# Kernel optimization log

Hardware: AMD Instinct MI355X
Metric: run time of the kernel (lower is better)

## Reference

```python
import jax, jax.numpy as jnp
import numpy as np

N, E, D_IN, D_H, D_OUT = 50000, 640000, 128, 128, 64
EPS = 1e-5


def _sage(x, src, dst, Wl, bl, Wr):
    # PyG SAGEConv: out = lin_l(mean_{j in N(i)} x_j) + lin_r(x_i)
    msg = x[src]                                             # [E, d] gather
    agg = jax.ops.segment_sum(msg, dst, num_segments=x.shape[0])
    deg = jax.ops.segment_sum(jnp.ones((src.shape[0],), x.dtype), dst,
                              num_segments=x.shape[0])
    agg = agg / jnp.maximum(deg, 1.0)[:, None]               # mean aggregate
    return agg @ Wl + bl + x @ Wr


def _bn_eval(x, gamma, beta, mean, var):
    return (x - mean) * jax.lax.rsqrt(var + EPS) * gamma + beta


def setup_inputs() -> dict:
    key = jax.random.key(0)
    ks = jax.random.split(key, 16)
    s = lambda d: 1.0 / np.sqrt(d)
    inp = {
        "x": jax.random.normal(ks[0], (N, D_IN), jnp.float32),
        "edge_index": jax.random.randint(ks[1], (2, E), 0, N, jnp.int64),
        # layer 0: 128 -> 128
        "Wl0": jax.random.normal(ks[2], (D_IN, D_H), jnp.float32) * s(D_IN),
        "bl0": jnp.zeros((D_H,), jnp.float32),
        "Wr0": jax.random.normal(ks[3], (D_IN, D_H), jnp.float32) * s(D_IN),
        # layer 1: 128 -> 128
        "Wl1": jax.random.normal(ks[4], (D_H, D_H), jnp.float32) * s(D_H),
        "bl1": jnp.zeros((D_H,), jnp.float32),
        "Wr1": jax.random.normal(ks[5], (D_H, D_H), jnp.float32) * s(D_H),
        # layer 2: 128 -> 64
        "Wl2": jax.random.normal(ks[6], (D_H, D_OUT), jnp.float32) * s(D_H),
        "bl2": jnp.zeros((D_OUT,), jnp.float32),
        "Wr2": jax.random.normal(ks[7], (D_H, D_OUT), jnp.float32) * s(D_H),
        # BatchNorm (eval mode) for the two hidden layers
        "g0": jnp.ones((D_H,), jnp.float32),
        "b0": jnp.zeros((D_H,), jnp.float32),
        "m0": jax.random.normal(ks[8], (D_H,), jnp.float32) * 0.1,
        "v0": jax.random.uniform(ks[9], (D_H,), jnp.float32, 0.5, 1.5),
        "g1": jnp.ones((D_H,), jnp.float32),
        "b1": jnp.zeros((D_H,), jnp.float32),
        "m1": jax.random.normal(ks[10], (D_H,), jnp.float32) * 0.1,
        "v1": jax.random.uniform(ks[11], (D_H,), jnp.float32, 0.5, 1.5),
    }
    return inp


def reference(x, edge_index, Wl0, bl0, Wr0, Wl1, bl1, Wr1, Wl2, bl2, Wr2,
              g0, b0, m0, v0, g1, b1, m1, v1):
    src, dst = edge_index[0], edge_index[1]
    # edge mask (edge_index < N) is all-true by construction -> no-op
    h = _sage(x, src, dst, Wl0, bl0, Wr0)
    h = jax.nn.relu(_bn_eval(h, g0, b0, m0, v0))   # eval: dropout is identity
    h = _sage(h, src, dst, Wl1, bl1, Wr1)
    h = jax.nn.relu(_bn_eval(h, g1, b1, m1, v1))
    h = _sage(h, src, dst, Wl2, bl2, Wr2)
    return jax.nn.log_softmax(h, axis=1)
```

## Files before the change

### kernel.cpp

```cpp
#include <hip/hip_runtime.h>

#define EPS 1e-5f
#define ELL_CAP 64
#define CNT_STRIDE 16

typedef __attribute__((ext_vector_type(8))) short short8;
typedef __attribute__((ext_vector_type(4))) float f32x4;

__device__ inline unsigned short f2b(float f) {
    union { float f; unsigned u; } v; v.f = f;
    unsigned u = v.u;
    return (unsigned short)((u + 0x7fffu + ((u >> 16) & 1u)) >> 16);
}
__device__ inline float b2f(unsigned short u) {
    union { unsigned u; float f; } v;
    v.u = ((unsigned)u) << 16;
    return v.f;
}


__device__ inline void cvt_one(const float* Wl, const float* Wr,
                               unsigned short* BT, int dout, int idx) {
    int n = idx >> 7, k = idx & 127;
    float w = (n < dout) ? Wl[k * dout + n] : Wr[k * dout + (n - dout)];
    BT[idx] = f2b(w);
}

__global__ void k_cvt_w3(const float* __restrict__ Wl0, const float* __restrict__ Wr0,
                         const float* __restrict__ Wl1, const float* __restrict__ Wr1,
                         const float* __restrict__ Wl2, const float* __restrict__ Wr2,
                         unsigned short* __restrict__ BT0,
                         unsigned short* __restrict__ BT1,
                         unsigned short* __restrict__ BT2) {
    int idx = blockIdx.x * blockDim.x + threadIdx.x;
    const int S0 = 256 * 128, S1 = 256 * 128, S2 = 128 * 128;
    if (idx < S0) cvt_one(Wl0, Wr0, BT0, 128, idx);
    else if (idx < S0 + S1) cvt_one(Wl1, Wr1, BT1, 128, idx - S0);
    else if (idx < S0 + S1 + S2) cvt_one(Wl2, Wr2, BT2, 64, idx - S0 - S1);
}


__device__ inline short8 pack8(float4 a, float4 b) {
    short8 r;
    r[0] = (short)f2b(a.x); r[1] = (short)f2b(a.y);
    r[2] = (short)f2b(a.z); r[3] = (short)f2b(a.w);
    r[4] = (short)f2b(b.x); r[5] = (short)f2b(b.y);
    r[6] = (short)f2b(b.z); r[7] = (short)f2b(b.w);
    return r;
}

template <int NCOLS, bool A32>
__device__ inline void gemm_body(unsigned short* Bs,
                                 const void* __restrict__ Av,
                                 const unsigned short* __restrict__ BT,
                                 unsigned short* __restrict__ C,
                                 int M, int bx, int by) {
    const int tid  = threadIdx.x;
    const int lane = tid & 63;
    const int wave = tid >> 6;
    const int m16  = lane & 15;
    const int q    = lane >> 4;
    const int row0 = (bx * 4 + wave) * 16;
    const int col0 = by * 128;

#pragma unroll
    for (int i = 0; i < 8; ++i) {
        int f   = tid + i * 256;
        int t   = f >> 8;
        int kc  = (f >> 6) & 3;
        int ln  = f & 63;
        int bm  = ln & 15, bq = ln >> 4;
        const short8* gp = (const short8*)(BT + (size_t)(col0 + t * 16 + bm) * 128
                                              + kc * 32 + bq * 8);
        *(short8*)(Bs + (size_t)f * 8) = *gp;
    }

    int arow = row0 + m16;
    if (arow >= M) arow = M - 1;
    short8 af0, af1, af2, af3;
    if (A32) {
        const float4* Ap = (const float4*)((const float*)Av + (size_t)arow * 128 + q * 8);
        af0 = pack8(Ap[0],  Ap[1]);
        af1 = pack8(Ap[8],  Ap[9]);
        af2 = pack8(Ap[16], Ap[17]);
        af3 = pack8(Ap[24], Ap[25]);
    } else {
        const short8* Ap = (const short8*)((const unsigned short*)Av + (size_t)arow * 128 + q * 8);
        af0 = Ap[0]; af1 = Ap[4]; af2 = Ap[8]; af3 = Ap[12];
    }

    __syncthreads();

    f32x4 acc[8] = {};
#pragma unroll
    for (int t = 0; t < 8; ++t) {
        const short8* bp = (const short8*)(Bs + (size_t)(t * 4) * 64 * 8 + (size_t)lane * 8);
        short8 b0 = bp[0];
        short8 b1 = bp[64];
        short8 b2 = bp[128];
        short8 b3 = bp[192];
        acc[t] = __builtin_amdgcn_mfma_f32_16x16x32_bf16(af0, b0, acc[t], 0, 0, 0);
        acc[t] = __builtin_amdgcn_mfma_f32_16x16x32_bf16(af1, b1, acc[t], 0, 0, 0);
        acc[t] = __builtin_amdgcn_mfma_f32_16x16x32_bf16(af2, b2, acc[t], 0, 0, 0);
        acc[t] = __builtin_amdgcn_mfma_f32_16x16x32_bf16(af3, b3, acc[t], 0, 0, 0);
    }

#pragma unroll
    for (int r = 0; r < 4; ++r) {
        int row = row0 + q * 4 + r;
        if (row < M) {
            unsigned short* cp = C + (size_t)row * NCOLS + col0 + m16;
#pragma unroll
            for (int t = 0; t < 8; ++t) cp[t * 16] = f2b(acc[t][r]);
        }
    }
}

template <int NCOLS, bool A32>
__global__ void k_mgemm_lds(const void* __restrict__ Av,
                            const unsigned short* __restrict__ BT,
                            unsigned short* __restrict__ C, int M) {
    __shared__ __align__(16) unsigned short Bs[8 * 4 * 64 * 8];
    gemm_body<NCOLS, A32>(Bs, Av, BT, C, M, blockIdx.x, blockIdx.y);
}


__global__ void k_mega(const int* __restrict__ src, const int* __restrict__ dst,
                       int E, int* __restrict__ cnt, unsigned short* __restrict__ ell,
                       int buildBlocks,
                       const float* __restrict__ x,
                       const unsigned short* __restrict__ BT0,
                       unsigned short* __restrict__ PQ, int M) {
    __shared__ __align__(16) unsigned short Bs[8 * 4 * 64 * 8];

    if ((int)blockIdx.x < buildBlocks) {
        int i = blockIdx.x * blockDim.x + threadIdx.x;
        int T = buildBlocks * blockDim.x;
        int e0 = i, e1 = i + T, e2 = i + 2 * T, e3 = i + 3 * T;
        int d0 = 0, d1 = 0, d2 = 0, d3 = 0;
        int s0 = 0, s1 = 0, s2 = 0, s3 = 0;
        if (e0 < E) { d0 = dst[e0]; s0 = src[e0]; }
        if (e1 < E) { d1 = dst[e1]; s1 = src[e1]; }
        if (e2 < E) { d2 = dst[e2]; s2 = src[e2]; }
        if (e3 < E) { d3 = dst[e3]; s3 = src[e3]; }
        int p0 = 0, p1 = 0, p2 = 0, p3 = 0;
        if (e0 < E) p0 = atomicAdd(&cnt[(size_t)d0 * CNT_STRIDE], 1);
        if (e1 < E) p1 = atomicAdd(&cnt[(size_t)d1 * CNT_STRIDE], 1);
        if (e2 < E) p2 = atomicAdd(&cnt[(size_t)d2 * CNT_STRIDE], 1);
        if (e3 < E) p3 = atomicAdd(&cnt[(size_t)d3 * CNT_STRIDE], 1);
        if (e0 < E && p0 < ELL_CAP) ell[(size_t)d0 * ELL_CAP + p0] = (unsigned short)s0;
        if (e1 < E && p1 < ELL_CAP) ell[(size_t)d1 * ELL_CAP + p1] = (unsigned short)s1;
        if (e2 < E && p2 < ELL_CAP) ell[(size_t)d2 * ELL_CAP + p2] = (unsigned short)s2;
        if (e3 < E && p3 < ELL_CAP) ell[(size_t)d3 * ELL_CAP + p3] = (unsigned short)s3;
        return;
    }
    int bid = blockIdx.x - buildBlocks;
    gemm_body<256, true>(Bs, x, BT0, PQ, M, bid >> 1, bid & 1);
}


__global__ void k_agg128(const unsigned short* __restrict__ PQ,
                         const int* __restrict__ cnt,
                         const unsigned short* __restrict__ ell,
                         const float* __restrict__ bl,
                         const float* __restrict__ g, const float* __restrict__ b,
                         const float* __restrict__ m, const float* __restrict__ v,
                         unsigned short* __restrict__ out, int n) {
    int node = (blockIdx.x * blockDim.x + threadIdx.x) >> 6;
    int lane = threadIdx.x & 63;
    if (node >= n) return;
    int cn  = cnt[(size_t)node * CNT_STRIDE];
    int deg = min(cn, ELL_CAP);
    int myidx = (lane < deg) ? (int)ell[(size_t)node * ELL_CAP + lane] : 0;
    const int half = lane >> 5, hl = lane & 31;

    float a0 = 0.f, a1 = 0.f, a2 = 0.f, a3 = 0.f;
    int j = 0;
    for (; j + 4 <= deg; j += 4) {
        int ia = __shfl(myidx, j + half);
        int ib = __shfl(myidx, j + 2 + half);
        ushort4 pa = *(const ushort4*)(PQ + (size_t)ia * 256 + 4 * hl);
        ushort4 pb = *(const ushort4*)(PQ + (size_t)ib * 256 + 4 * hl);
        a0 += b2f(pa.x) + b2f(pb.x);
        a1 += b2f(pa.y) + b2f(pb.y);
        a2 += b2f(pa.z) + b2f(pb.z);
        a3 += b2f(pa.w) + b2f(pb.w);
    }
    for (; j < deg; j += 2) {
        int rem = deg - j;
        int ia = __shfl(myidx, min(j + half, deg - 1));
        if (half == 0 || rem >= 2) {
            ushort4 pa = *(const ushort4*)(PQ + (size_t)ia * 256 + 4 * hl);
            a0 += b2f(pa.x); a1 += b2f(pa.y); a2 += b2f(pa.z); a3 += b2f(pa.w);
        }
    }
    a0 += __shfl_xor(a0, 32);
    a1 += __shfl_xor(a1, 32);
    a2 += __shfl_xor(a2, 32);
    a3 += __shfl_xor(a3, 32);

    float dg = fmaxf((float)cn, 1.f);
    ushort4 qv = *(const ushort4*)(PQ + (size_t)node * 256 + 128 + 4 * hl);
    int c0 = 4 * hl;
    float4 blv = *(const float4*)(bl + c0);
    float4 mv  = *(const float4*)(m + c0);
    float4 vv  = *(const float4*)(v + c0);
    float4 gv  = *(const float4*)(g + c0);
    float4 bv  = *(const float4*)(b + c0);
    float z0 = (a0 / dg + b2f(qv.x) + blv.x - mv.x) * rsqrtf(vv.x + EPS) * gv.x + bv.x;
    float z1 = (a1 / dg + b2f(qv.y) + blv.y - mv.y) * rsqrtf(vv.y + EPS) * gv.y + bv.y;
    float z2 = (a2 / dg + b2f(qv.z) + blv.z - mv.z) * rsqrtf(vv.z + EPS) * gv.z + bv.z;
    float z3 = (a3 / dg + b2f(qv.w) + blv.w - mv.w) * rsqrtf(vv.w + EPS) * gv.w + bv.w;
    if (half == 0) {
        ushort4 r;
        r.x = f2b(fmaxf(z0, 0.f));
        r.y = f2b(fmaxf(z1, 0.f));
        r.z = f2b(fmaxf(z2, 0.f));
        r.w = f2b(fmaxf(z3, 0.f));
        *(ushort4*)(out + (size_t)node * 128 + c0) = r;
    }
}


__global__ void k_agg64(const unsigned short* __restrict__ PQ,
                        const int* __restrict__ cnt,
                        const unsigned short* __restrict__ ell,
                        const float* __restrict__ bl,
                        float* __restrict__ out, int n) {
    int node = (blockIdx.x * blockDim.x + threadIdx.x) >> 6;
    int lane = threadIdx.x & 63;
    if (node >= n) return;
    int cn  = cnt[(size_t)node * CNT_STRIDE];
    int deg = min(cn, ELL_CAP);
    int myidx = (lane < deg) ? (int)ell[(size_t)node * ELL_CAP + lane] : 0;
    const int qtr = lane >> 4, ql = lane & 15;

    float a0 = 0.f, a1 = 0.f, a2 = 0.f, a3 = 0.f;
    int j = 0;
    for (; j + 8 <= deg; j += 8) {
        int ia = __shfl(myidx, j + qtr);
        int ib = __shfl(myidx, j + 4 + qtr);
        ushort4 pa = *(const ushort4*)(PQ + (size_t)ia * 128 + 4 * ql);
        ushort4 pb = *(const ushort4*)(PQ + (size_t)ib * 128 + 4 * ql);
        a0 += b2f(pa.x) + b2f(pb.x);
        a1 += b2f(pa.y) + b2f(pb.y);
        a2 += b2f(pa.z) + b2f(pb.z);
        a3 += b2f(pa.w) + b2f(pb.w);
    }
    for (; j < deg; j += 4) {
        int rem = deg - j;
        int ia = __shfl(myidx, min(j + qtr, deg - 1));
        if (qtr < rem) {
            ushort4 pa = *(const ushort4*)(PQ + (size_t)ia * 128 + 4 * ql);
            a0 += b2f(pa.x); a1 += b2f(pa.y); a2 += b2f(pa.z); a3 += b2f(pa.w);
        }
    }
    a0 += __shfl_xor(a0, 16); a0 += __shfl_xor(a0, 32);
    a1 += __shfl_xor(a1, 16); a1 += __shfl_xor(a1, 32);
    a2 += __shfl_xor(a2, 16); a2 += __shfl_xor(a2, 32);
    a3 += __shfl_xor(a3, 16); a3 += __shfl_xor(a3, 32);

    float dg = fmaxf((float)cn, 1.f);
    ushort4 qv = *(const ushort4*)(PQ + (size_t)node * 128 + 64 + 4 * ql);
    int c0 = 4 * ql;
    float4 blv = *(const float4*)(bl + c0);
    float z0 = a0 / dg + b2f(qv.x) + blv.x;
    float z1 = a1 / dg + b2f(qv.y) + blv.y;
    float z2 = a2 / dg + b2f(qv.z) + blv.z;
    float z3 = a3 / dg + b2f(qv.w) + blv.w;

    float mx = fmaxf(fmaxf(z0, z1), fmaxf(z2, z3));
#pragma unroll
    for (int off = 8; off > 0; off >>= 1) mx = fmaxf(mx, __shfl_xor(mx, off));
    float sm = __expf(z0 - mx) + __expf(z1 - mx) + __expf(z2 - mx) + __expf(z3 - mx);
#pragma unroll
    for (int off = 8; off > 0; off >>= 1) sm += __shfl_xor(sm, off);
    float lg = mx + __logf(sm);
    if (qtr == 0) {
        float4 o = make_float4(z0 - lg, z1 - lg, z2 - lg, z3 - lg);
        *(float4*)(out + (size_t)node * 64 + c0) = o;
    }
}


extern "C" void kernel_launch(void* const* d_in, const int* in_sizes, int n_in,
                              void* d_out, int out_size, void* d_ws, size_t ws_size,
                              hipStream_t stream) {
    const float* x   = (const float*)d_in[0];
    const int*   ei  = (const int*)d_in[1];
    const float* Wl0 = (const float*)d_in[2];
    const float* bl0 = (const float*)d_in[3];
    const float* Wr0 = (const float*)d_in[4];
    const float* Wl1 = (const float*)d_in[5];
    const float* bl1 = (const float*)d_in[6];
    const float* Wr1 = (const float*)d_in[7];
    const float* Wl2 = (const float*)d_in[8];
    const float* bl2 = (const float*)d_in[9];
    const float* Wr2 = (const float*)d_in[10];
    const float* g0  = (const float*)d_in[11];
    const float* b0  = (const float*)d_in[12];
    const float* m0  = (const float*)d_in[13];
    const float* v0  = (const float*)d_in[14];
    const float* g1  = (const float*)d_in[15];
    const float* b1  = (const float*)d_in[16];
    const float* m1  = (const float*)d_in[17];
    const float* v1  = (const float*)d_in[18];

    const int N = in_sizes[0] / 128;
    const int E = in_sizes[1] / 2;
    const int* src = ei;
    const int* dst = ei + E;

    size_t off = 0;
    auto alloc = [&](size_t bytes) -> void* {
        void* p = (char*)d_ws + off;
        off += (bytes + 255) & ~(size_t)255;
        return p;
    };
    int* cnt = (int*)alloc((size_t)N * CNT_STRIDE * 4);
    unsigned short* ell = (unsigned short*)alloc((size_t)N * ELL_CAP * 2);
    unsigned short* PQ  = (unsigned short*)alloc((size_t)N * 256 * 2);
    unsigned short* hb  = (unsigned short*)alloc((size_t)N * 128 * 2);
    unsigned short* BT0 = (unsigned short*)alloc((size_t)256 * 128 * 2);
    unsigned short* BT1 = (unsigned short*)alloc((size_t)256 * 128 * 2);
    unsigned short* BT2 = (unsigned short*)alloc((size_t)128 * 128 * 2);
    (void)ws_size;

    hipMemsetAsync(cnt, 0, (size_t)N * CNT_STRIDE * 4, stream);
    const int CVT_TOTAL = 256 * 128 + 256 * 128 + 128 * 128;
    k_cvt_w3<<<(CVT_TOTAL + 255) / 256, 256, 0, stream>>>(
        Wl0, Wr0, Wl1, Wr1, Wl2, Wr2, BT0, BT1, BT2);

    int rowBlocks = (N + 63) / 64;
    dim3 mg2(rowBlocks, 2);
    dim3 mg1(rowBlocks, 1);
    int aggGrid = (N + 3) / 4;

    int buildBlocks = ((E + 3) / 4 + 255) / 256;
    int gemmBlocks  = rowBlocks * 2;
    k_mega<<<buildBlocks + gemmBlocks, 256, 0, stream>>>(
        src, dst, E, cnt, ell, buildBlocks, x, BT0, PQ, N);

    k_agg128<<<aggGrid, 256, 0, stream>>>(PQ, cnt, ell, bl0, g0, b0, m0, v0, hb, N);
    k_mgemm_lds<256, false><<<mg2, 256, 0, stream>>>(hb, BT1, PQ, N);
    k_agg128<<<aggGrid, 256, 0, stream>>>(PQ, cnt, ell, bl1, g1, b1, m1, v1, hb, N);
    k_mgemm_lds<128, false><<<mg1, 256, 0, stream>>>(hb, BT2, PQ, N);
    k_agg64<<<aggGrid, 256, 0, stream>>>(PQ, cnt, ell, bl2, (float*)d_out, N);
}
```

Before: 261.4 us.

## Fuse all stages into one persistent cooperative kernel with grid syncs

Replaces the chain of separate launches (memset, weight conversion, ELL build plus first GEMM, aggregations and GEMMs) with a single persistent cooperative kernel. The grid is sized to occupancy and uses grid.sync between stages, with grid-stride loops over tiles and nodes. The goal is to remove per-launch overhead and tail gaps between the small kernels. In exchange it limits concurrency to one resident wave of blocks per stage, adds grid-barrier cost, and the ELL build runs on only an eighth of the blocks. A multi-kernel fallback remains if the cooperative launch fails.

```diff
diff --git a/kernel.cpp b/kernel.cpp
--- a/kernel.cpp
+++ b/kernel.cpp
@@ -1,8 +1,12 @@
 #include <hip/hip_runtime.h>
+#include <hip/hip_cooperative_groups.h>
+
+namespace cg = cooperative_groups;
 
 #define EPS 1e-5f
 #define ELL_CAP 64
 #define CNT_STRIDE 16
+#define BLK 256
 
 typedef __attribute__((ext_vector_type(8))) short short8;
 typedef __attribute__((ext_vector_type(4))) float f32x4;
@@ -17,7 +21,6 @@
     v.u = ((unsigned)u) << 16;
     return v.f;
 }
-
 
 __device__ inline void cvt_one(const float* Wl, const float* Wr,
                                unsigned short* BT, int dout, int idx) {
@@ -25,20 +28,6 @@
     float w = (n < dout) ? Wl[k * dout + n] : Wr[k * dout + (n - dout)];
     BT[idx] = f2b(w);
 }
-
-__global__ void k_cvt_w3(const float* __restrict__ Wl0, const float* __restrict__ Wr0,
-                         const float* __restrict__ Wl1, const float* __restrict__ Wr1,
-                         const float* __restrict__ Wl2, const float* __restrict__ Wr2,
-                         unsigned short* __restrict__ BT0,
-                         unsigned short* __restrict__ BT1,
-                         unsigned short* __restrict__ BT2) {
-    int idx = blockIdx.x * blockDim.x + threadIdx.x;
-    const int S0 = 256 * 128, S1 = 256 * 128, S2 = 128 * 128;
-    if (idx < S0) cvt_one(Wl0, Wr0, BT0, 128, idx);
-    else if (idx < S0 + S1) cvt_one(Wl1, Wr1, BT1, 128, idx - S0);
-    else if (idx < S0 + S1 + S2) cvt_one(Wl2, Wr2, BT2, 64, idx - S0 - S1);
-}
-
 
 __device__ inline short8 pack8(float4 a, float4 b) {
     short8 r;
@@ -49,8 +38,9 @@
     return r;
 }
 
+
 template <int NCOLS, bool A32>
-__device__ inline void gemm_body(unsigned short* Bs,
+__device__ inline void gemm_tile(unsigned short* Bs,
                                  const void* __restrict__ Av,
                                  const unsigned short* __restrict__ BT,
                                  unsigned short* __restrict__ C,
@@ -114,61 +104,18 @@
             for (int t = 0; t < 8; ++t) cp[t * 16] = f2b(acc[t][r]);
         }
     }
-}
-
-template <int NCOLS, bool A32>
-__global__ void k_mgemm_lds(const void* __restrict__ Av,
-                            const unsigned short* __restrict__ BT,
-                            unsigned short* __restrict__ C, int M) {
-    __shared__ __align__(16) unsigned short Bs[8 * 4 * 64 * 8];
-    gemm_body<NCOLS, A32>(Bs, Av, BT, C, M, blockIdx.x, blockIdx.y);
-}
-
-
-__global__ void k_mega(const int* __restrict__ src, const int* __restrict__ dst,
-                       int E, int* __restrict__ cnt, unsigned short* __restrict__ ell,
-                       int buildBlocks,
-                       const float* __restrict__ x,
-                       const unsigned short* __restrict__ BT0,
-                       unsigned short* __restrict__ PQ, int M) {
-    __shared__ __align__(16) unsigned short Bs[8 * 4 * 64 * 8];
-
-    if ((int)blockIdx.x < buildBlocks) {
-        int i = blockIdx.x * blockDim.x + threadIdx.x;
-        int T = buildBlocks * blockDim.x;
-        int e0 = i, e1 = i + T, e2 = i + 2 * T, e3 = i + 3 * T;
-        int d0 = 0, d1 = 0, d2 = 0, d3 = 0;
-        int s0 = 0, s1 = 0, s2 = 0, s3 = 0;
-        if (e0 < E) { d0 = dst[e0]; s0 = src[e0]; }
-        if (e1 < E) { d1 = dst[e1]; s1 = src[e1]; }
-        if (e2 < E) { d2 = dst[e2]; s2 = src[e2]; }
-        if (e3 < E) { d3 = dst[e3]; s3 = src[e3]; }
-        int p0 = 0, p1 = 0, p2 = 0, p3 = 0;
-        if (e0 < E) p0 = atomicAdd(&cnt[(size_t)d0 * CNT_STRIDE], 1);
-        if (e1 < E) p1 = atomicAdd(&cnt[(size_t)d1 * CNT_STRIDE], 1);
-        if (e2 < E) p2 = atomicAdd(&cnt[(size_t)d2 * CNT_STRIDE], 1);
-        if (e3 < E) p3 = atomicAdd(&cnt[(size_t)d3 * CNT_STRIDE], 1);
-        if (e0 < E && p0 < ELL_CAP) ell[(size_t)d0 * ELL_CAP + p0] = (unsigned short)s0;
-        if (e1 < E && p1 < ELL_CAP) ell[(size_t)d1 * ELL_CAP + p1] = (unsigned short)s1;
-        if (e2 < E && p2 < ELL_CAP) ell[(size_t)d2 * ELL_CAP + p2] = (unsigned short)s2;
-        if (e3 < E && p3 < ELL_CAP) ell[(size_t)d3 * ELL_CAP + p3] = (unsigned short)s3;
-        return;
-    }
-    int bid = blockIdx.x - buildBlocks;
-    gemm_body<256, true>(Bs, x, BT0, PQ, M, bid >> 1, bid & 1);
-}
-
-
-__global__ void k_agg128(const unsigned short* __restrict__ PQ,
-                         const int* __restrict__ cnt,
-                         const unsigned short* __restrict__ ell,
-                         const float* __restrict__ bl,
-                         const float* __restrict__ g, const float* __restrict__ b,
-                         const float* __restrict__ m, const float* __restrict__ v,
-                         unsigned short* __restrict__ out, int n) {
-    int node = (blockIdx.x * blockDim.x + threadIdx.x) >> 6;
-    int lane = threadIdx.x & 63;
-    if (node >= n) return;
+    __syncthreads();
+}
+
+
+__device__ inline void agg128_node(const unsigned short* __restrict__ PQ,
+                                   const int* __restrict__ cnt,
+                                   const unsigned short* __restrict__ ell,
+                                   const float* __restrict__ bl,
+                                   const float* __restrict__ g, const float* __restrict__ b,
+                                   const float* __restrict__ m, const float* __restrict__ v,
+                                   unsigned short* __restrict__ out,
+                                   int node, int lane) {
     int cn  = cnt[(size_t)node * CNT_STRIDE];
     int deg = min(cn, ELL_CAP);
     int myidx = (lane < deg) ? (int)ell[(size_t)node * ELL_CAP + lane] : 0;
@@ -221,15 +168,12 @@
     }
 }
 
-
-__global__ void k_agg64(const unsigned short* __restrict__ PQ,
-                        const int* __restrict__ cnt,
-                        const unsigned short* __restrict__ ell,
-                        const float* __restrict__ bl,
-                        float* __restrict__ out, int n) {
-    int node = (blockIdx.x * blockDim.x + threadIdx.x) >> 6;
-    int lane = threadIdx.x & 63;
-    if (node >= n) return;
+__device__ inline void agg64_node(const unsigned short* __restrict__ PQ,
+                                  const int* __restrict__ cnt,
+                                  const unsigned short* __restrict__ ell,
+                                  const float* __restrict__ bl,
+                                  float* __restrict__ out,
+                                  int node, int lane) {
     int cn  = cnt[(size_t)node * CNT_STRIDE];
     int deg = min(cn, ELL_CAP);
     int myidx = (lane < deg) ? (int)ell[(size_t)node * ELL_CAP + lane] : 0;
@@ -283,33 +227,156 @@
 }
 
 
+struct KParams {
+    const float* x; const int* src; const int* dst;
+    const float *Wl0, *Wr0, *Wl1, *Wr1, *Wl2, *Wr2;
+    const float *bl0, *bl1, *bl2;
+    const float *g0, *b0, *m0, *v0, *g1, *b1, *m1, *v1;
+    int N, E, buildBlocks;
+    int* cnt;
+    unsigned short *ell, *PQ, *hb, *BT0, *BT1, *BT2;
+    float* out;
+};
+
+
+__global__ void __launch_bounds__(BLK, 4) k_all(KParams p) {
+    __shared__ __align__(16) unsigned short Bs[8 * 4 * 64 * 8];
+    cg::grid_group grid = cg::this_grid();
+
+    const int nblk = gridDim.x;
+    const int tid  = threadIdx.x;
+    const int gtid = blockIdx.x * BLK + tid;
+    const int GT   = nblk * BLK;
+    const int lane = tid & 63;
+    const int wgid = blockIdx.x * 4 + (tid >> 6);
+    const int wstr = nblk * 4;
+    const int rowBlocks = (p.N + 63) >> 6;
+
+    const int CZ = p.N * CNT_STRIDE;
+    for (int i = gtid; i < CZ; i += GT) p.cnt[i] = 0;
+    {
+        const int S0 = 256 * 128, S1 = 256 * 128, S2 = 128 * 128;
+        for (int idx = gtid; idx < S0 + S1 + S2; idx += GT) {
+            if (idx < S0) cvt_one(p.Wl0, p.Wr0, p.BT0, 128, idx);
+            else if (idx < S0 + S1) cvt_one(p.Wl1, p.Wr1, p.BT1, 128, idx - S0);
+            else cvt_one(p.Wl2, p.Wr2, p.BT2, 64, idx - S0 - S1);
+        }
+    }
+    grid.sync();
+
+    const int bb = p.buildBlocks;
+    if ((int)blockIdx.x < bb) {
+        const int T = bb * BLK;
+        int i = blockIdx.x * BLK + tid;
+        for (int base = 0; base < p.E; base += 4 * T) {
+            int e0 = base + i, e1 = e0 + T, e2 = e1 + T, e3 = e2 + T;
+            int d0 = 0, d1 = 0, d2 = 0, d3 = 0;
+            int s0 = 0, s1 = 0, s2 = 0, s3 = 0;
+            if (e0 < p.E) { d0 = p.dst[e0]; s0 = p.src[e0]; }
+            if (e1 < p.E) { d1 = p.dst[e1]; s1 = p.src[e1]; }
+            if (e2 < p.E) { d2 = p.dst[e2]; s2 = p.src[e2]; }
+            if (e3 < p.E) { d3 = p.dst[e3]; s3 = p.src[e3]; }
+            int p0 = 0, p1 = 0, p2 = 0, p3 = 0;
+            if (e0 < p.E) p0 = atomicAdd(&p.cnt[(size_t)d0 * CNT_STRIDE], 1);
+            if (e1 < p.E) p1 = atomicAdd(&p.cnt[(size_t)d1 * CNT_STRIDE], 1);
+            if (e2 < p.E) p2 = atomicAdd(&p.cnt[(size_t)d2 * CNT_STRIDE], 1);
+            if (e3 < p.E) p3 = atomicAdd(&p.cnt[(size_t)d3 * CNT_STRIDE], 1);
+            if (e0 < p.E && p0 < ELL_CAP) p.ell[(size_t)d0 * ELL_CAP + p0] = (unsigned short)s0;
+            if (e1 < p.E && p1 < ELL_CAP) p.ell[(size_t)d1 * ELL_CAP + p1] = (unsigned short)s1;
+            if (e2 < p.E && p2 < ELL_CAP) p.ell[(size_t)d2 * ELL_CAP + p2] = (unsigned short)s2;
+            if (e3 < p.E && p3 < ELL_CAP) p.ell[(size_t)d3 * ELL_CAP + p3] = (unsigned short)s3;
+        }
+    } else {
+        const int nt = rowBlocks * 2;
+        for (int t = blockIdx.x - bb; t < nt; t += nblk - bb)
+            gemm_tile<256, true>(Bs, p.x, p.BT0, p.PQ, p.N, t >> 1, t & 1);
+    }
+    grid.sync();
+
+    for (int node = wgid; node < p.N; node += wstr)
+        agg128_node(p.PQ, p.cnt, p.ell, p.bl0, p.g0, p.b0, p.m0, p.v0, p.hb, node, lane);
+    grid.sync();
+
+    {
+        const int nt = rowBlocks * 2;
+        for (int t = blockIdx.x; t < nt; t += nblk)
+            gemm_tile<256, false>(Bs, p.hb, p.BT1, p.PQ, p.N, t >> 1, t & 1);
+    }
+    grid.sync();
+
+    for (int node = wgid; node < p.N; node += wstr)
+        agg128_node(p.PQ, p.cnt, p.ell, p.bl1, p.g1, p.b1, p.m1, p.v1, p.hb, node, lane);
+    grid.sync();
+
+    for (int t = blockIdx.x; t < rowBlocks; t += nblk)
+        gemm_tile<128, false>(Bs, p.hb, p.BT2, p.PQ, p.N, t, 0);
+    grid.sync();
+
+    for (int node = wgid; node < p.N; node += wstr)
+        agg64_node(p.PQ, p.cnt, p.ell, p.bl2, p.out, node, lane);
+}
+
+
+__global__ void k_prep(KParams p) {
+    int idx = blockIdx.x * blockDim.x + threadIdx.x;
+    int GT = gridDim.x * blockDim.x;
+    for (int i = idx; i < p.N * CNT_STRIDE; i += GT) p.cnt[i] = 0;
+    const int S0 = 256 * 128, S1 = 256 * 128, S2 = 128 * 128;
+    for (int i = idx; i < S0 + S1 + S2; i += GT) {
+        if (i < S0) cvt_one(p.Wl0, p.Wr0, p.BT0, 128, i);
+        else if (i < S0 + S1) cvt_one(p.Wl1, p.Wr1, p.BT1, 128, i - S0);
+        else cvt_one(p.Wl2, p.Wr2, p.BT2, 64, i - S0 - S1);
+    }
+}
+
+__global__ void k_build_ell(KParams p) {
+    int i = blockIdx.x * blockDim.x + threadIdx.x;
+    int T = gridDim.x * blockDim.x;
+    int e0 = i, e1 = i + T, e2 = i + 2 * T, e3 = i + 3 * T;
+    int d0 = 0, d1 = 0, d2 = 0, d3 = 0;
+    int s0 = 0, s1 = 0, s2 = 0, s3 = 0;
+    if (e0 < p.E) { d0 = p.dst[e0]; s0 = p.src[e0]; }
+    if (e1 < p.E) { d1 = p.dst[e1]; s1 = p.src[e1]; }
+    if (e2 < p.E) { d2 = p.dst[e2]; s2 = p.src[e2]; }
+    if (e3 < p.E) { d3 = p.dst[e3]; s3 = p.src[e3]; }
+    int p0 = 0, p1 = 0, p2 = 0, p3 = 0;
+    if (e0 < p.E) p0 = atomicAdd(&p.cnt[(size_t)d0 * CNT_STRIDE], 1);
+    if (e1 < p.E) p1 = atomicAdd(&p.cnt[(size_t)d1 * CNT_STRIDE], 1);
+    if (e2 < p.E) p2 = atomicAdd(&p.cnt[(size_t)d2 * CNT_STRIDE], 1);
+    if (e3 < p.E) p3 = atomicAdd(&p.cnt[(size_t)d3 * CNT_STRIDE], 1);
+    if (e0 < p.E && p0 < ELL_CAP) p.ell[(size_t)d0 * ELL_CAP + p0] = (unsigned short)s0;
+    if (e1 < p.E && p1 < ELL_CAP) p.ell[(size_t)d1 * ELL_CAP + p1] = (unsigned short)s1;
+    if (e2 < p.E && p2 < ELL_CAP) p.ell[(size_t)d2 * ELL_CAP + p2] = (unsigned short)s2;
+    if (e3 < p.E && p3 < ELL_CAP) p.ell[(size_t)d3 * ELL_CAP + p3] = (unsigned short)s3;
+}
+
+template <int NCOLS, bool A32>
+__global__ void k_mgemm_lds(const void* __restrict__ Av,
+                            const unsigned short* __restrict__ BT,
+                            unsigned short* __restrict__ C, int M) {
+    __shared__ __align__(16) unsigned short Bs[8 * 4 * 64 * 8];
+    gemm_tile<NCOLS, A32>(Bs, Av, BT, C, M, blockIdx.x, blockIdx.y);
+}
+
+__global__ void k_agg128w(KParams p, const float* bl, const float* g, const float* b,
+                          const float* m, const float* v) {
+    int node = (blockIdx.x * blockDim.x + threadIdx.x) >> 6;
+    if (node >= p.N) return;
+    agg128_node(p.PQ, p.cnt, p.ell, bl, g, b, m, v, p.hb, node, threadIdx.x & 63);
+}
+
+__global__ void k_agg64w(KParams p) {
+    int node = (blockIdx.x * blockDim.x + threadIdx.x) >> 6;
+    if (node >= p.N) return;
+    agg64_node(p.PQ, p.cnt, p.ell, p.bl2, p.out, node, threadIdx.x & 63);
+}
+
+
 extern "C" void kernel_launch(void* const* d_in, const int* in_sizes, int n_in,
                               void* d_out, int out_size, void* d_ws, size_t ws_size,
                               hipStream_t stream) {
-    const float* x   = (const float*)d_in[0];
-    const int*   ei  = (const int*)d_in[1];
-    const float* Wl0 = (const float*)d_in[2];
-    const float* bl0 = (const float*)d_in[3];
-    const float* Wr0 = (const float*)d_in[4];
-    const float* Wl1 = (const float*)d_in[5];
-    const float* bl1 = (const float*)d_in[6];
-    const float* Wr1 = (const float*)d_in[7];
-    const float* Wl2 = (const float*)d_in[8];
-    const float* bl2 = (const float*)d_in[9];
-    const float* Wr2 = (const float*)d_in[10];
-    const float* g0  = (const float*)d_in[11];
-    const float* b0  = (const float*)d_in[12];
-    const float* m0  = (const float*)d_in[13];
-    const float* v0  = (const float*)d_in[14];
-    const float* g1  = (const float*)d_in[15];
-    const float* b1  = (const float*)d_in[16];
-    const float* m1  = (const float*)d_in[17];
-    const float* v1  = (const float*)d_in[18];
-
     const int N = in_sizes[0] / 128;
     const int E = in_sizes[1] / 2;
-    const int* src = ei;
-    const int* dst = ei + E;
 
     size_t off = 0;
     auto alloc = [&](size_t bytes) -> void* {
@@ -326,24 +393,57 @@
     unsigned short* BT2 = (unsigned short*)alloc((size_t)128 * 128 * 2);
     (void)ws_size;
 
-    hipMemsetAsync(cnt, 0, (size_t)N * CNT_STRIDE * 4, stream);
-    const int CVT_TOTAL = 256 * 128 + 256 * 128 + 128 * 128;
-    k_cvt_w3<<<(CVT_TOTAL + 255) / 256, 256, 0, stream>>>(
-        Wl0, Wr0, Wl1, Wr1, Wl2, Wr2, BT0, BT1, BT2);
+    KParams p;
+    p.x   = (const float*)d_in[0];
+    p.src = (const int*)d_in[1];
+    p.dst = (const int*)d_in[1] + E;
+    p.Wl0 = (const float*)d_in[2];  p.bl0 = (const float*)d_in[3];
+    p.Wr0 = (const float*)d_in[4];
+    p.Wl1 = (const float*)d_in[5];  p.bl1 = (const float*)d_in[6];
+    p.Wr1 = (const float*)d_in[7];
+    p.Wl2 = (const float*)d_in[8];  p.bl2 = (const float*)d_in[9];
+    p.Wr2 = (const float*)d_in[10];
+    p.g0 = (const float*)d_in[11]; p.b0 = (const float*)d_in[12];
+    p.m0 = (const float*)d_in[13]; p.v0 = (const float*)d_in[14];
+    p.g1 = (const float*)d_in[15]; p.b1 = (const float*)d_in[16];
+    p.m1 = (const float*)d_in[17]; p.v1 = (const float*)d_in[18];
+    p.N = N; p.E = E; p.buildBlocks = 1;
+    p.cnt = cnt; p.ell = ell; p.PQ = PQ; p.hb = hb;
+    p.BT0 = BT0; p.BT1 = BT1; p.BT2 = BT2;
+    p.out = (float*)d_out;
+
+    int maxB = 0;
+    hipError_t oe = hipOccupancyMaxActiveBlocksPerMultiprocessor(
+        &maxB, (const void*)k_all, BLK, 0);
+    int numCU = 0;
+    {
+        hipDeviceProp_t prop;
+        int dev = 0;
+        if (hipGetDevice(&dev) == hipSuccess &&
+            hipGetDeviceProperties(&prop, dev) == hipSuccess)
+            numCU = prop.multiProcessorCount;
+    }
+    hipError_t le = hipErrorUnknown;
+    if (oe == hipSuccess && maxB > 0 && numCU > 0) {
+        int grid = maxB * numCU;
+        int bbv = grid / 8; if (bbv < 1) bbv = 1; if (bbv > grid - 1) bbv = grid - 1;
+        p.buildBlocks = bbv;
+        void* args[] = { &p };
+        le = hipLaunchCooperativeKernel((void*)k_all, dim3(grid), dim3(BLK), args, 0, stream);
+    }
+    if (le == hipSuccess) return;
 
     int rowBlocks = (N + 63) / 64;
     dim3 mg2(rowBlocks, 2);
     dim3 mg1(rowBlocks, 1);
     int aggGrid = (N + 3) / 4;
 
-    int buildBlocks = ((E + 3) / 4 + 255) / 256;
-    int gemmBlocks  = rowBlocks * 2;
-    k_mega<<<buildBlocks + gemmBlocks, 256, 0, stream>>>(
-        src, dst, E, cnt, ell, buildBlocks, x, BT0, PQ, N);
-
-    k_agg128<<<aggGrid, 256, 0, stream>>>(PQ, cnt, ell, bl0, g0, b0, m0, v0, hb, N);
-    k_mgemm_lds<256, false><<<mg2, 256, 0, stream>>>(hb, BT1, PQ, N);
-    k_agg128<<<aggGrid, 256, 0, stream>>>(PQ, cnt, ell, bl1, g1, b1, m1, v1, hb, N);
-    k_mgemm_lds<128, false><<<mg1, 256, 0, stream>>>(hb, BT2, PQ, N);
-    k_agg64<<<aggGrid, 256, 0, stream>>>(PQ, cnt, ell, bl2, (float*)d_out, N);
-}
+    k_prep<<<512, BLK, 0, stream>>>(p);
+    k_build_ell<<<((E + 3) / 4 + BLK - 1) / BLK, BLK, 0, stream>>>(p);
+    k_mgemm_lds<256, true><<<mg2, BLK, 0, stream>>>(p.x, BT0, PQ, N);
+    k_agg128w<<<aggGrid, BLK, 0, stream>>>(p, p.bl0, p.g0, p.b0, p.m0, p.v0);
+    k_mgemm_lds<256, false><<<mg2, BLK, 0, stream>>>(hb, BT1, PQ, N);
+    k_agg128w<<<aggGrid, BLK, 0, stream>>>(p, p.bl1, p.g1, p.b1, p.m1, p.v1);
+    k_mgemm_lds<128, false><<<mg1, BLK, 0, stream>>>(hb, BT2, PQ, N);
+    k_agg64w<<<aggGrid, BLK, 0, stream>>>(p);
+}
```

Result: slower. 765.5 us (+192.8%).
